# Optimization experiments

Measured on AMD Instinct MI355X. Metric: run time of the kernel, lower is better.

## Reference

```python
import jax, jax.numpy as jnp
import numpy as np
from jax import lax

RO = 4.0            # snake_config.ro (feature-map downsample ratio)
N_ADJ = 4           # snake_config.adj_num -> kernel = 2*4+1 = 9
K = 2 * N_ADJ + 1
DIL = (1, 1, 1, 2, 2, 4, 4)   # dilations of the 7 Snake residual circular convs
NMS_RADIUS = 2      # radius used in the iterative refinement cls_nms


def circ_conv(x, w, b, d):
    """Dilated circular conv along polygon axis. x:[N,C,P], w:[O,I,K]."""
    pad = N_ADJ * d
    xp = jnp.concatenate([x[..., -pad:], x, x[..., :pad]], axis=-1)
    y = lax.conv_general_dilated(xp, w, window_strides=(1,), padding='VALID',
                                 rhs_dilation=(d,),
                                 dimension_numbers=('NCH', 'OIH', 'NCH'))
    return y + b[None, :, None]


def conv1x1(x, w, b):
    # x:[N,C,P], w:[O,C] -> [N,O,P]
    return jnp.einsum('ncp,oc->nop', x, w) + b[None, :, None]


def bilinear_gather(cnn_feature, poly, ind):
    """grid_sample-style bilinear sampling (align_corners=False, zero pad).
    cnn_feature:[B,C,H,W], poly:[N,P,2] pixel coords, ind:[N] image index.
    Returns [N,C,P]."""
    B, C, H, W = cnn_feature.shape
    x = poly[..., 0] - 0.5
    y = poly[..., 1] - 0.5
    x0 = jnp.floor(x); y0 = jnp.floor(y)
    wx = x - x0; wy = y - y0
    x0i = x0.astype(jnp.int32); y0i = y0.astype(jnp.int32)

    def tap(yi, xi):
        valid = (xi >= 0) & (xi < W) & (yi >= 0) & (yi < H)
        xi_c = jnp.clip(xi, 0, W - 1)
        yi_c = jnp.clip(yi, 0, H - 1)
        f = cnn_feature[ind[:, None], :, yi_c, xi_c]  # [N,P,C]
        return f * valid[..., None]

    f00 = tap(y0i, x0i);     f01 = tap(y0i, x0i + 1)
    f10 = tap(y0i + 1, x0i); f11 = tap(y0i + 1, x0i + 1)
    out = (f00 * ((1 - wx) * (1 - wy))[..., None]
           + f01 * (wx * (1 - wy))[..., None]
           + f10 * ((1 - wx) * wy)[..., None]
           + f11 * (wx * wy)[..., None])
    return out.transpose(0, 2, 1)  # [N,C,P]


def cls_nms(cls, radius):
    """Circular local-max suppression of per-vertex scores. cls:[N,P,1]."""
    c = cls[..., 0]
    m = jnp.max(jnp.stack([jnp.roll(c, s, axis=1)
                           for s in range(-radius, radius + 1)], 0), axis=0)
    return jnp.where(c >= m, c, 0.0)[..., None]


def snake_body(x, head_w, head_b, res_w, res_b, fusion_w, fusion_b,
               pred1_w, pred1_b, pred2_w, pred2_b, pred3_w, pred3_b,
               cls1_w, cls1_b, cls2_w, cls2_b, cls3_w, cls3_b):
    h = jax.nn.relu(circ_conv(x, head_w, head_b, 1))
    states = [h]
    for i in range(7):  # fixed 7 residual layers, structurally distinct dilations
        r = jax.nn.relu(circ_conv(states[-1], res_w[i], res_b[i], DIL[i]))
        states.append(r + states[-1])
    state = jnp.concatenate(states, axis=1)                 # [N, 8*128, P]
    g = conv1x1(state, fusion_w, fusion_b)                  # [N, 256, P]
    g = jnp.max(g, axis=2, keepdims=True)
    g = jnp.broadcast_to(g, (state.shape[0], g.shape[1], state.shape[2]))
    state = jnp.concatenate([g, state], axis=1)             # [N, 1280, P]

    def head3(w1, b1, w2, b2, w3, b3):
        h1 = jax.nn.relu(conv1x1(state, w1, b1))
        h2 = jax.nn.relu(conv1x1(h1, w2, b2))
        return conv1x1(h2, w3, b3)

    offset = head3(pred1_w, pred1_b, pred2_w, pred2_b, pred3_w, pred3_b)  # [N,2,P]
    cls = head3(cls1_w, cls1_b, cls2_w, cls2_b, cls3_w, cls3_b)           # [N,1,P]
    return offset, cls


def setup_inputs() -> dict:
    key = jax.random.key(0)
    ks = jax.random.split(key, 32)
    B, C, H, W = 4, 64, 128, 128
    N, P = 512, 128
    SD = 128  # state_dim
    FD = 64 + 2 + 1  # feature_dim for iterative evolve_gcn
    std = 0.01  # conv init: normal(0, 0.01), bias 0 (matches module init)
    inp = {
        'cnn_feature': jax.random.normal(ks[0], (B, C, H, W), jnp.float32),
        'i_it_py': jax.random.uniform(ks[1], (N, P, 2), jnp.float32) * (W - 1),
        'c_it_py': jax.random.normal(ks[2], (N, P, 2), jnp.float32) * 0.2,
        'it_cls': jax.random.uniform(ks[3], (N, P), jnp.float32),
        'ind': jax.random.randint(ks[4], (N,), 0, B, jnp.int32),
        'head_w': jax.random.normal(ks[5], (SD, FD, K), jnp.float32) * std,
        'head_b': jnp.zeros((SD,), jnp.float32),
        'res_w': jax.random.normal(ks[6], (7, SD, SD, K), jnp.float32) * std,
        'res_b': jnp.zeros((7, SD), jnp.float32),
        'fusion_w': jax.random.normal(ks[7], (256, 8 * SD), jnp.float32) * std,
        'fusion_b': jnp.zeros((256,), jnp.float32),
        'pred1_w': jax.random.normal(ks[8], (256, 8 * SD + 256), jnp.float32) * std,
        'pred1_b': jnp.zeros((256,), jnp.float32),
        'pred2_w': jax.random.normal(ks[9], (64, 256), jnp.float32) * std,
        'pred2_b': jnp.zeros((64,), jnp.float32),
        'pred3_w': jax.random.normal(ks[10], (2, 64), jnp.float32) * std,
        'pred3_b': jnp.zeros((2,), jnp.float32),
        'cls1_w': jax.random.normal(ks[11], (256, 8 * SD + 256), jnp.float32) * std,
        'cls1_b': jnp.zeros((256,), jnp.float32),
        'cls2_w': jax.random.normal(ks[12], (64, 256), jnp.float32) * std,
        'cls2_b': jnp.zeros((64,), jnp.float32),
        'cls3_w': jax.random.normal(ks[13], (1, 64), jnp.float32) * std,
        'cls3_b': jnp.zeros((1,), jnp.float32),
    }
    return inp


def reference(cnn_feature, i_it_py, c_it_py, it_cls, ind,
              head_w, head_b, res_w, res_b, fusion_w, fusion_b,
              pred1_w, pred1_b, pred2_w, pred2_b, pred3_w, pred3_b,
              cls1_w, cls1_b, cls2_w, cls2_b, cls3_w, cls3_b):
    # evolve_poly: gather CNN features at vertices, concat scaled canonical
    # coords + per-vertex cls, run Snake, add offsets, NMS sigmoid scores.
    feat = bilinear_gather(cnn_feature, i_it_py, ind)        # [N,64,P]
    c = (c_it_py * RO).transpose(0, 2, 1)                    # [N,2,P]
    x = jnp.concatenate([feat, c, it_cls[:, None, :]], axis=1)  # [N,67,P]
    offset, cls = snake_body(x, head_w, head_b, res_w, res_b, fusion_w, fusion_b,
                             pred1_w, pred1_b, pred2_w, pred2_b, pred3_w, pred3_b,
                             cls1_w, cls1_b, cls2_w, cls2_b, cls3_w, cls3_b)
    i_poly = i_it_py * RO + offset.transpose(0, 2, 1)        # [N,P,2]
    cls = cls.transpose(0, 2, 1)                             # [N,P,1]
    nms = cls_nms(jax.nn.sigmoid(cls), NMS_RADIUS)           # [N,P,1]
    return i_poly, cls, nms
```

## Files before the change

kernel.cpp:

```cpp
#include <hip/hip_runtime.h>
#include <math.h>

typedef __attribute__((ext_vector_type(8))) short bf16x8;
typedef __attribute__((ext_vector_type(4))) float f32x4;

#define UOFF_CAW 0L
#define UOFF_FAW 2359296L
#define UOFF_H1W 2883584L
#define UOFF_W2F 3932160L
#define NB_TOT   3997696L
#define OFF_W1G  1998848L
#define OFF_GRAW 2129920L
#define OFF_DYN  2260992L
#define REPACK_N 4128768L

__device__ inline ushort f2bf_rne(float x) {
  uint u = __float_as_uint(x);
  return (ushort)((u + 0x7FFFu + ((u >> 16) & 1u)) >> 16);
}
__device__ inline void split_bf(float x, ushort& h, ushort& l) {
  uint u = __float_as_uint(x);
  uint hb = (u + 0x7FFFu + ((u >> 16) & 1u)) & 0xFFFF0000u;
  h = (ushort)(hb >> 16);
  l = f2bf_rne(x - __uint_as_float(hb));
}
__device__ inline ushort bfsel(float w, int split) {
  uint u = __float_as_uint(w);
  uint hb = (u + 0x7FFFu + ((u >> 16) & 1u)) & 0xFFFF0000u;
  if (split == 0) return (ushort)(hb >> 16);
  float lo = w - __uint_as_float(hb);
  uint ul = __float_as_uint(lo);
  return (ushort)((ul + 0x7FFFu + ((ul >> 16) & 1u)) >> 16);
}
__device__ inline bf16x8 asb(uint4 a) {
  union { uint4 u; bf16x8 v; } x; x.u = a; return x.v;
}
__device__ inline f32x4 MFMA_(bf16x8 a, bf16x8 b, f32x4 c) {
  return __builtin_amdgcn_mfma_f32_16x16x32_bf16(a, b, c, 0, 0, 0);
}
__device__ inline void bar_lgkm() {
  asm volatile("s_waitcnt lgkmcnt(0)" ::: "memory");
  __builtin_amdgcn_s_barrier();
}

__device__ inline void read_frag_pair(const char* xb, int pc, int g, int ic,
                                      bf16x8& bh, bf16x8& bl) {
  const int s0 = (pc & 7) << 4;
  const char* a = xb + pc * 512 + (((ic * 64 + (g << 4))) ^ s0);
  bh = asb(*(const uint4*)a);
  bl = asb(*(const uint4*)(a + 256));
}

__global__ void k_repack(const float* __restrict__ head_w, const float* __restrict__ res_w,
                         const float* __restrict__ fusion_w,
                         const float* __restrict__ pred1_w, const float* __restrict__ cls1_w,
                         const float* __restrict__ pred2_w, const float* __restrict__ cls2_w,
                         float* __restrict__ ws) {
  const long j = (long)blockIdx.x * 256 + threadIdx.x;
  if (j >= REPACK_N) return;
  if (j < NB_TOT) {
    ushort* wsu = (ushort*)ws;
    float w;
    if (j < UOFF_FAW) {
      int e = (int)(j & 7); long q = j >> 3;
      int lane = (int)(q & 63); q >>= 6;
      int mt = (int)(q & 1); q >>= 1;
      int split = (int)(q & 1); q >>= 1;
      int ic = (int)(q & 3); q >>= 2;
      int tap = (int)(q % 9); q /= 9;
      int mp = (int)(q & 3); int l = (int)(q >> 2);
      int gg = lane >> 4;
      int kl = (e < 4) ? (4 * gg + e) : (16 + 4 * gg + e - 4);
      int m = mp * 32 + mt * 16 + (lane & 15);
      int i = ic * 32 + kl;
      if (l == 0) w = (i < 67) ? head_w[((long)m * 67 + i) * 9 + tap] : 0.f;
      else        w = res_w[(((long)(l - 1) * 128 + m) * 128 + i) * 9 + tap];
      wsu[j] = bfsel(w, split);
    } else if (j < UOFF_H1W) {
      long jj = j - UOFF_FAW;
      int e = (int)(jj & 7); long q = jj >> 3;
      int lane = (int)(q & 63); q >>= 6;
      int mt = (int)(q & 1); q >>= 1;
      int split = (int)(q & 1); q >>= 1;
      int ic = (int)(q & 3); q >>= 2;
      int fm2 = (int)(q & 7); int l = (int)(q >> 3);
      int gg = lane >> 4;
      int kl = (e < 4) ? (4 * gg + e) : (16 + 4 * gg + e - 4);
      int m = fm2 * 32 + mt * 16 + (lane & 15);
      int i = ic * 32 + kl;
      w = fusion_w[(long)m * 1024 + l * 128 + i];
      wsu[j] = bfsel(w, split);
    } else if (j < UOFF_W2F) {
      long jj = j - UOFF_H1W;
      int e = (int)(jj & 7); long q = jj >> 3;
      int lane = (int)(q & 63); q >>= 6;
      int mt = (int)(q & 1); q >>= 1;
      int split = (int)(q & 1); q >>= 1;
      int ic = (int)(q & 3); q >>= 2;
      int slab = (int)(q & 7); q >>= 3;
      int mp = (int)(q & 7); int blk = (int)(q >> 3);
      int gg = lane >> 4;
      int kl = (e < 4) ? (4 * gg + e) : (16 + 4 * gg + e - 4);
      int m = blk * 256 + mp * 32 + mt * 16 + (lane & 15);
      int k = slab * 128 + ic * 32 + kl;
      w = (m < 256) ? pred1_w[(long)m * 1280 + 256 + k] : cls1_w[(long)(m - 256) * 1280 + 256 + k];
      wsu[j] = bfsel(w, split);
    } else {
      long jj = j - UOFF_W2F;
      int e = (int)(jj & 7); long q = jj >> 3;
      int lane = (int)(q & 63); q >>= 6;
      int split = (int)(q & 1); q >>= 1;
      int ic = (int)(q & 7); q >>= 3;
      int mfr = (int)(q & 3); int blk = (int)(q >> 2);
      int gg = lane >> 4;
      int kl = (e < 4) ? (4 * gg + e) : (16 + 4 * gg + e - 4);
      int m = mfr * 16 + (lane & 15);
      int k = ic * 32 + kl;
      w = blk ? cls2_w[(long)m * 256 + k] : pred2_w[(long)m * 256 + k];
      wsu[j] = bfsel(w, split);
    }
  } else {
    long q = j - NB_TOT; int o = (int)(q & 511); int c = (int)(q >> 9);
    ws[OFF_W1G + q] = (o < 256) ? pred1_w[(long)o * 1280 + c] : cls1_w[(long)(o - 256) * 1280 + c];
  }
}

__global__ __launch_bounds__(1024) __attribute__((amdgpu_waves_per_eu(4)))
void k_conv(const float* __restrict__ cnn, const float* __restrict__ i_it,
            const float* __restrict__ c_it, const float* __restrict__ cls_in,
            const int* __restrict__ ind,
            const ushort* __restrict__ CAW, const ushort* __restrict__ FAW,
            const float* __restrict__ head_b, const float* __restrict__ res_b,
            float* __restrict__ graw, float* __restrict__ states, int p0) {
  __shared__ uint4 xt4[4096];
  __shared__ float scr[512];
  char* xb = (char*)xt4;
  const int ln = blockIdx.x, n = p0 + ln, t = threadIdx.x;
  const int lane = t & 63, li = lane & 15, g = lane >> 4;
  const int wv = __builtin_amdgcn_readfirstlane(t >> 6);
  const int mp = wv & 3, np = wv >> 2;
  const int fm2 = wv & 7, fq = wv >> 3;

  {
    const int p = t & 127, qg = t >> 7;
    const long nb = (long)n * 128 + p;
    const int sw = p & 7;
    if (qg < 4) {
      const float gx = i_it[nb * 2 + 0] - 0.5f;
      const float gy = i_it[nb * 2 + 1] - 0.5f;
      const float fx = floorf(gx), fy = floorf(gy);
      const float wx = gx - fx, wy = gy - fy;
      const int x0 = (int)fx, y0 = (int)fy, x1 = x0 + 1, y1 = y0 + 1;
      const bool vx0 = (x0 >= 0) & (x0 < 128), vx1 = (x1 >= 0) & (x1 < 128);
      const bool vy0 = (y0 >= 0) & (y0 < 128), vy1 = (y1 >= 0) & (y1 < 128);
      const int x0c = min(max(x0, 0), 127), x1c = min(max(x1, 0), 127);
      const int y0c = min(max(y0, 0), 127), y1c = min(max(y1, 0), 127);
      const float w00 = (vx0 && vy0) ? (1.f - wx) * (1.f - wy) : 0.f;
      const float w01 = (vx1 && vy0) ? wx * (1.f - wy) : 0.f;
      const float w10 = (vx0 && vy1) ? (1.f - wx) * wy : 0.f;
      const float w11 = (vx1 && vy1) ? wx * wy : 0.f;
      const long base = (long)ind[n] * (64L * 16384);
      const int a00 = y0c * 128 + x0c, a01 = y0c * 128 + x1c;
      const int a10 = y1c * 128 + x0c, a11 = y1c * 128 + x1c;
#pragma unroll
      for (int qq = 0; qq < 4; qq++) {
        ushort hh[4], ll[4];
#pragma unroll
        for (int cc = 0; cc < 4; cc++) {
          const int c = qg * 16 + qq * 4 + cc;
          const float* f = cnn + base + (long)c * 16384;
          float x = f[a00] * w00 + f[a01] * w01 + f[a10] * w10 + f[a11] * w11;
          split_bf(x, hh[cc], ll[cc]);
        }
        const int G = ((qg >> 1) * 4 + qq) ^ sw;
        char* a = xb + p * 512 + G * 16 + (qg & 1) * 8;
        *(uint2*)a = make_uint2((uint)hh[0] | ((uint)hh[1] << 16), (uint)hh[2] | ((uint)hh[3] << 16));
        *(uint2*)(a + 256) = make_uint2((uint)ll[0] | ((uint)ll[1] << 16), (uint)ll[2] | ((uint)ll[3] << 16));
      }
    } else {
#pragma unroll
      for (int qq = 0; qq < 4; qq++) {
        ushort hh[4], ll[4];
        if (qg == 4 && qq == 0) {
          float v0 = c_it[nb * 2 + 0] * 4.f, v1 = c_it[nb * 2 + 1] * 4.f, v2 = cls_in[nb];
          split_bf(v0, hh[0], ll[0]); split_bf(v1, hh[1], ll[1]); split_bf(v2, hh[2], ll[2]);
          hh[3] = 0; ll[3] = 0;
        } else {
          hh[0] = hh[1] = hh[2] = hh[3] = 0; ll[0] = ll[1] = ll[2] = ll[3] = 0;
        }
        const int G = ((qg >> 1) * 4 + qq) ^ sw;
        char* a = xb + p * 512 + G * 16 + (qg & 1) * 8;
        *(uint2*)a = make_uint2((uint)hh[0] | ((uint)hh[1] << 16), (uint)hh[2] | ((uint)hh[3] << 16));
        *(uint2*)(a + 256) = make_uint2((uint)ll[0] | ((uint)ll[1] << 16), (uint)ll[2] | ((uint)ll[3] << 16));
      }
    }
  }
  __syncthreads();

  const f32x4 fz = {0.f, 0.f, 0.f, 0.f};
  f32x4 facc[2][4];
#pragma unroll
  for (int a = 0; a < 2; a++)
#pragma unroll
    for (int b = 0; b < 4; b++) facc[a][b] = fz;

  const uint4* caw = (const uint4*)CAW;
  const uint4* faw = (const uint4*)FAW;
  uint4* stq = (uint4*)(states + (long)ln * 131072);

  for (int l = 0; l < 8; l++) {
    const int dil = (l >= 6) ? 4 : ((l >= 4) ? 2 : 1);
    const int nic = (l == 0) ? 3 : 4;
    if (l > 0) {
      uint4* dst = stq + (long)(l - 1) * 4096;
#pragma unroll
      for (int k = 0; k < 4; k++) dst[k * 1024 + t] = xt4[k * 1024 + t];
      const uint4* fawl = faw + ((long)((l - 1) * 8 + fm2)) * 1024 + lane;
#pragma unroll
      for (int ic = 0; ic < 4; ic++) {
        const uint4* w0 = fawl + ic * 256;
        const bf16x8 Ah0 = asb(w0[0]),   Ah1 = asb(w0[64]);
        const bf16x8 Al0 = asb(w0[128]), Al1 = asb(w0[192]);
#pragma unroll
        for (int nt = 0; nt < 4; nt++) {
          const int pc = fq * 64 + nt * 16 + li;
          bf16x8 bh, bl;
          read_frag_pair(xb, pc, g, ic, bh, bl);
          facc[0][nt] = MFMA_(Ah0, bh, facc[0][nt]);
          facc[1][nt] = MFMA_(Ah1, bh, facc[1][nt]);
          facc[0][nt] = MFMA_(Ah0, bl, facc[0][nt]);
          facc[1][nt] = MFMA_(Ah1, bl, facc[1][nt]);
          facc[0][nt] = MFMA_(Al0, bh, facc[0][nt]);
          facc[1][nt] = MFMA_(Al1, bh, facc[1][nt]);
        }
      }
    }
    f32x4 cacc[2][2];
    cacc[0][0] = fz; cacc[0][1] = fz; cacc[1][0] = fz; cacc[1][1] = fz;
    const uint4* cawl = caw + ((long)(l * 4 + mp)) * 9216;
    for (int tap = 0; tap < 9; tap++) {
      const int shift = (tap - 4) * dil;
      const int pc0 = (np * 32 + li + shift + 128) & 127;
      const int pc1 = (np * 32 + 16 + li + shift + 128) & 127;
      const uint4* cawt = cawl + tap * 1024 + lane;
      for (int ic = 0; ic < nic; ic++) {
        bf16x8 bh0, bl0, bh1, bl1;
        read_frag_pair(xb, pc0, g, ic, bh0, bl0);
        read_frag_pair(xb, pc1, g, ic, bh1, bl1);
        const uint4* w0 = cawt + ic * 256;
        const bf16x8 Ah0 = asb(w0[0]),   Ah1 = asb(w0[64]);
        const bf16x8 Al0 = asb(w0[128]), Al1 = asb(w0[192]);
        cacc[0][0] = MFMA_(Ah0, bh0, cacc[0][0]);
        cacc[0][1] = MFMA_(Ah0, bh1, cacc[0][1]);
        cacc[1][0] = MFMA_(Ah1, bh0, cacc[1][0]);
        cacc[1][1] = MFMA_(Ah1, bh1, cacc[1][1]);
        cacc[0][0] = MFMA_(Ah0, bl0, cacc[0][0]);
        cacc[0][1] = MFMA_(Ah0, bl1, cacc[0][1]);
        cacc[1][0] = MFMA_(Ah1, bl0, cacc[1][0]);
        cacc[1][1] = MFMA_(Ah1, bl1, cacc[1][1]);
        cacc[0][0] = MFMA_(Al0, bh0, cacc[0][0]);
        cacc[0][1] = MFMA_(Al0, bh1, cacc[0][1]);
        cacc[1][0] = MFMA_(Al1, bh0, cacc[1][0]);
        cacc[1][1] = MFMA_(Al1, bh1, cacc[1][1]);
      }
    }
    bar_lgkm();
    {
      const float* bsrc = (l == 0) ? head_b : (res_b + (l - 1) * 128);
      const float4 b0 = *(const float4*)&bsrc[mp * 32 + g * 4];
      const float4 b1 = *(const float4*)&bsrc[mp * 32 + 16 + g * 4];
#pragma unroll
      for (int nt = 0; nt < 2; nt++) {
        const int p = np * 32 + nt * 16 + li;
        const int X = (mp * 64 + g * 16) ^ ((p & 7) << 4);
        char* a = xb + p * 512 + X;
        float v[8];
        v[0] = fmaxf(cacc[0][nt][0] + b0.x, 0.f);
        v[1] = fmaxf(cacc[0][nt][1] + b0.y, 0.f);
        v[2] = fmaxf(cacc[0][nt][2] + b0.z, 0.f);
        v[3] = fmaxf(cacc[0][nt][3] + b0.w, 0.f);
        v[4] = fmaxf(cacc[1][nt][0] + b1.x, 0.f);
        v[5] = fmaxf(cacc[1][nt][1] + b1.y, 0.f);
        v[6] = fmaxf(cacc[1][nt][2] + b1.z, 0.f);
        v[7] = fmaxf(cacc[1][nt][3] + b1.w, 0.f);
        if (l > 0) {
          const uint4 oh = *(const uint4*)a;
          const uint4 ol = *(const uint4*)(a + 256);
          const uint hw[4] = {oh.x, oh.y, oh.z, oh.w};
          const uint lw[4] = {ol.x, ol.y, ol.z, ol.w};
#pragma unroll
          for (int k = 0; k < 8; k++) {
            const uint hh = (k & 1) ? (hw[k >> 1] & 0xFFFF0000u) : ((hw[k >> 1] & 0xFFFFu) << 16);
            const uint ll = (k & 1) ? (lw[k >> 1] & 0xFFFF0000u) : ((lw[k >> 1] & 0xFFFFu) << 16);
            v[k] += __uint_as_float(hh) + __uint_as_float(ll);
          }
        }
        ushort hh[8], ll[8];
#pragma unroll
        for (int k = 0; k < 8; k++) split_bf(v[k], hh[k], ll[k]);
        *(uint4*)a = make_uint4((uint)hh[0] | ((uint)hh[1] << 16), (uint)hh[2] | ((uint)hh[3] << 16),
                                (uint)hh[4] | ((uint)hh[5] << 16), (uint)hh[6] | ((uint)hh[7] << 16));
        *(uint4*)(a + 256) = make_uint4((uint)ll[0] | ((uint)ll[1] << 16), (uint)ll[2] | ((uint)ll[3] << 16),
                                        (uint)ll[4] | ((uint)ll[5] << 16), (uint)ll[6] | ((uint)ll[7] << 16));
      }
    }
    __syncthreads();
  }

  {
    uint4* dst = stq + 7L * 4096;
#pragma unroll
    for (int k = 0; k < 4; k++) dst[k * 1024 + t] = xt4[k * 1024 + t];
    const uint4* fawl = faw + ((long)(7 * 8 + fm2)) * 1024 + lane;
#pragma unroll
    for (int ic = 0; ic < 4; ic++) {
      const uint4* w0 = fawl + ic * 256;
      const bf16x8 Ah0 = asb(w0[0]),   Ah1 = asb(w0[64]);
      const bf16x8 Al0 = asb(w0[128]), Al1 = asb(w0[192]);
#pragma unroll
      for (int nt = 0; nt < 4; nt++) {
        const int pc = fq * 64 + nt * 16 + li;
        bf16x8 bh, bl;
        read_frag_pair(xb, pc, g, ic, bh, bl);
        facc[0][nt] = MFMA_(Ah0, bh, facc[0][nt]);
        facc[1][nt] = MFMA_(Ah1, bh, facc[1][nt]);
        facc[0][nt] = MFMA_(Ah0, bl, facc[0][nt]);
        facc[1][nt] = MFMA_(Ah1, bl, facc[1][nt]);
        facc[0][nt] = MFMA_(Al0, bh, facc[0][nt]);
        facc[1][nt] = MFMA_(Al1, bh, facc[1][nt]);
      }
    }
  }

#pragma unroll
  for (int mt = 0; mt < 2; mt++) {
#pragma unroll
    for (int r = 0; r < 4; r++) {
      float m = fmaxf(fmaxf(facc[mt][0][r], facc[mt][1][r]),
                      fmaxf(facc[mt][2][r], facc[mt][3][r]));
#pragma unroll
      for (int s = 1; s < 16; s <<= 1) m = fmaxf(m, __shfl_xor(m, s, 64));
      if (li == 0) scr[(fm2 * 32 + mt * 16 + g * 4 + r) * 2 + fq] = m;
    }
  }
  bar_lgkm();
  if (t < 256) graw[(long)n * 256 + t] = fmaxf(scr[2 * t], scr[2 * t + 1]);
}

__global__ __launch_bounds__(1024) __attribute__((amdgpu_waves_per_eu(4)))
void k_h1t(const float* __restrict__ states, const ushort* __restrict__ H1W,
           const ushort* __restrict__ W2F,
           const float* __restrict__ graw, const float* __restrict__ fus_b,
           const float* __restrict__ W1G, const float* __restrict__ p1b, const float* __restrict__ c1b,
           const float* __restrict__ p2b, const float* __restrict__ c2b,
           const float* __restrict__ p3w, const float* __restrict__ p3b,
           const float* __restrict__ c3w, const float* __restrict__ c3b,
           const float* __restrict__ i_it, float* __restrict__ out, int p0) {
  __shared__ uint4 xt4[4096];
  __shared__ float sg[256];
  __shared__ float hg_s[256];
  char* xb = (char*)xt4;
  const int b = blockIdx.x, ln = b >> 1, blk = b & 1, t = threadIdx.x;
  const int n = p0 + ln;
  const int lane = t & 63, li = lane & 15, g = lane >> 4;
  const int wv = __builtin_amdgcn_readfirstlane(t >> 6);
  const int mw = wv & 7, qw = wv >> 3;
  const uint4* sp = (const uint4*)(states + (long)ln * 131072);
  const uint4* aw = (const uint4*)H1W;
  const uint4* w2 = (const uint4*)W2F;
  const f32x4 fz = {0.f, 0.f, 0.f, 0.f};

  uint4 stg[4];
#pragma unroll
  for (int k = 0; k < 4; k++) stg[k] = sp[k * 1024 + t];

  if (t < 256) sg[t] = graw[(long)n * 256 + t] + fus_b[t];
  __syncthreads();
  if (t < 256) {
    float s = blk ? c1b[t] : p1b[t];
    const float* w = W1G + blk * 256 + t;
#pragma unroll 8
    for (int c = 0; c < 256; c++) s = fmaf(w[(long)c * 512], sg[c], s);
    hg_s[t] = s;
  }

  f32x4 acc[2][4];
#pragma unroll
  for (int a = 0; a < 2; a++)
#pragma unroll
    for (int c = 0; c < 4; c++) acc[a][c] = fz;

  for (int s = 0; s < 8; s++) {
#pragma unroll
    for (int k = 0; k < 4; k++) xt4[k * 1024 + t] = stg[k];
    bar_lgkm();
    if (s < 7) {
#pragma unroll
      for (int k = 0; k < 4; k++) stg[k] = sp[(s + 1) * 4096 + k * 1024 + t];
    }
    const uint4* awl = aw + (((long)(blk * 8 + mw)) * 8 + s) * 1024 + lane;
#pragma unroll
    for (int ic = 0; ic < 4; ic++) {
      const uint4* w0 = awl + ic * 256;
      const bf16x8 Ah0 = asb(w0[0]),   Ah1 = asb(w0[64]);
      const bf16x8 Al0 = asb(w0[128]), Al1 = asb(w0[192]);
#pragma unroll
      for (int nt = 0; nt < 4; nt++) {
        const int pc = qw * 64 + nt * 16 + li;
        bf16x8 bh, bl;
        read_frag_pair(xb, pc, g, ic, bh, bl);
        acc[0][nt] = MFMA_(Ah0, bh, acc[0][nt]);
        acc[1][nt] = MFMA_(Ah1, bh, acc[1][nt]);
        acc[0][nt] = MFMA_(Ah0, bl, acc[0][nt]);
        acc[1][nt] = MFMA_(Ah1, bl, acc[1][nt]);
        acc[0][nt] = MFMA_(Al0, bh, acc[0][nt]);
        acc[1][nt] = MFMA_(Al1, bh, acc[1][nt]);
      }
    }
    bar_lgkm();
  }

  const float4 hq0 = *(const float4*)&hg_s[mw * 32 + g * 4];
  const float4 hq1 = *(const float4*)&hg_s[mw * 32 + 16 + g * 4];
#pragma unroll
  for (int nt = 0; nt < 4; nt++) {
    acc[0][nt][0] = fmaxf(acc[0][nt][0] + hq0.x, 0.f);
    acc[0][nt][1] = fmaxf(acc[0][nt][1] + hq0.y, 0.f);
    acc[0][nt][2] = fmaxf(acc[0][nt][2] + hq0.z, 0.f);
    acc[0][nt][3] = fmaxf(acc[0][nt][3] + hq0.w, 0.f);
    acc[1][nt][0] = fmaxf(acc[1][nt][0] + hq1.x, 0.f);
    acc[1][nt][1] = fmaxf(acc[1][nt][1] + hq1.y, 0.f);
    acc[1][nt][2] = fmaxf(acc[1][nt][2] + hq1.z, 0.f);
    acc[1][nt][3] = fmaxf(acc[1][nt][3] + hq1.w, 0.f);
  }

  const int mfr = wv & 3, nfr = wv >> 2;
  const float* b2 = blk ? c2b : p2b;
  f32x4 a2s[2];
#pragma unroll
  for (int h = 0; h < 2; h++) {
    bar_lgkm();
    if (qw == h) {
#pragma unroll
      for (int nt = 0; nt < 4; nt++) {
        const int pl = nt * 16 + li;
        char* a = xb + pl * 1024 + ((mw * 64 + g * 16) ^ ((pl & 7) << 4));
        ushort hh[8], ll[8];
#pragma unroll
        for (int e = 0; e < 4; e++) { split_bf(acc[0][nt][e], hh[e], ll[e]); }
#pragma unroll
        for (int e = 0; e < 4; e++) { split_bf(acc[1][nt][e], hh[4 + e], ll[4 + e]); }
        *(uint4*)a = make_uint4((uint)hh[0] | ((uint)hh[1] << 16), (uint)hh[2] | ((uint)hh[3] << 16),
                                (uint)hh[4] | ((uint)hh[5] << 16), (uint)hh[6] | ((uint)hh[7] << 16));
        *(uint4*)(a + 512) = make_uint4((uint)ll[0] | ((uint)ll[1] << 16), (uint)ll[2] | ((uint)ll[3] << 16),
                                        (uint)ll[4] | ((uint)ll[5] << 16), (uint)ll[6] | ((uint)ll[7] << 16));
      }
    }
    bar_lgkm();
    a2s[h] = fz;
    {
      const int pl = nfr * 16 + li;
#pragma unroll
      for (int ic = 0; ic < 8; ic++) {
        const uint4* wb = w2 + (((long)(blk * 4 + mfr) * 8 + ic) * 2) * 64 + lane;
        const bf16x8 Ah = asb(wb[0]), Al = asb(wb[64]);
        const char* ba = xb + pl * 1024 + ((ic * 64 + g * 16) ^ ((pl & 7) << 4));
        const bf16x8 bh = asb(*(const uint4*)ba);
        const bf16x8 bl = asb(*(const uint4*)(ba + 512));
        a2s[h] = MFMA_(Ah, bh, a2s[h]);
        a2s[h] = MFMA_(Ah, bl, a2s[h]);
        a2s[h] = MFMA_(Al, bh, a2s[h]);
      }
    }
  }
  bar_lgkm();

  {
    float* h2L = (float*)xb;
    const int jl = mfr * 16 + g * 4;
#pragma unroll
    for (int h = 0; h < 2; h++) {
      const int pos = h * 64 + nfr * 16 + li;
      h2L[(jl + 0) * 128 + pos] = fmaxf(a2s[h][0] + b2[jl + 0], 0.f);
      h2L[(jl + 1) * 128 + pos] = fmaxf(a2s[h][1] + b2[jl + 1], 0.f);
      h2L[(jl + 2) * 128 + pos] = fmaxf(a2s[h][2] + b2[jl + 2], 0.f);
      h2L[(jl + 3) * 128 + pos] = fmaxf(a2s[h][3] + b2[jl + 3], 0.f);
    }
  }
  bar_lgkm();

  {
    const float* h2L = (const float*)xb;
    const int pp = t & 127;
    if (blk == 0) {
      if (t < 128) {
        float o0v = p3b[0], o1v = p3b[1];
        for (int j = 0; j < 64; j++) {
          const float hp = h2L[j * 128 + pp];
          o0v = fmaf(p3w[j], hp, o0v);
          o1v = fmaf(p3w[64 + j], hp, o1v);
        }
        const long ip = ((long)n * 128 + pp) * 2;
        out[ip + 0] = i_it[ip + 0] * 4.f + o0v;
        out[ip + 1] = i_it[ip + 1] * 4.f + o1v;
      }
    } else {
      float sig = 0.f;
      if (t < 128) {
        float cv = c3b[0];
        for (int j = 0; j < 64; j++) cv = fmaf(c3w[j], h2L[j * 128 + pp], cv);
        out[131072 + (long)n * 128 + pp] = cv;
        sig = 1.f / (1.f + expf(-cv));
        sg[pp] = sig;
      }
      bar_lgkm();
      if (t < 128) {
        float m = sg[pp];
#pragma unroll
        for (int s = 1; s <= 2; s++) {
          m = fmaxf(m, sg[(pp + s) & 127]);
          m = fmaxf(m, sg[(pp + 128 - s) & 127]);
        }
        out[196608 + (long)n * 128 + pp] = (sig >= m) ? sig : 0.f;
      }
    }
  }
}

extern "C" void kernel_launch(void* const* d_in, const int* in_sizes, int n_in,
                              void* d_out, int out_size, void* d_ws, size_t ws_size,
                              hipStream_t stream) {
  const float* cnn      = (const float*)d_in[0];
  const float* i_it     = (const float*)d_in[1];
  const float* c_it     = (const float*)d_in[2];
  const float* it_cls   = (const float*)d_in[3];
  const int*   ind      = (const int*)d_in[4];
  const float* head_w   = (const float*)d_in[5];
  const float* head_b   = (const float*)d_in[6];
  const float* res_w    = (const float*)d_in[7];
  const float* res_b    = (const float*)d_in[8];
  const float* fusion_w = (const float*)d_in[9];
  const float* fusion_b = (const float*)d_in[10];
  const float* pred1_w  = (const float*)d_in[11];
  const float* pred1_b  = (const float*)d_in[12];
  const float* pred2_w  = (const float*)d_in[13];
  const float* pred2_b  = (const float*)d_in[14];
  const float* pred3_w  = (const float*)d_in[15];
  const float* pred3_b  = (const float*)d_in[16];
  const float* cls1_w   = (const float*)d_in[17];
  const float* cls1_b   = (const float*)d_in[18];
  const float* cls2_w   = (const float*)d_in[19];
  const float* cls2_b   = (const float*)d_in[20];
  const float* cls3_w   = (const float*)d_in[21];
  const float* cls3_b   = (const float*)d_in[22];
  float* ws = (float*)d_ws;
  float* out = (float*)d_out;
  const ushort* wsu = (const ushort*)d_ws;

  k_repack<<<(int)((REPACK_N + 255) / 256), 256, 0, stream>>>(
      head_w, res_w, fusion_w, pred1_w, cls1_w, pred2_w, cls2_w, ws);

  long avail_f = (long)(ws_size / 4) - OFF_DYN;
  long Cl = avail_f / 131072;
  int C = (Cl >= 512) ? 512 : ((Cl >= 256) ? 256 : (int)(Cl < 1 ? 1 : Cl));
  float* states = ws + OFF_DYN;

  for (int p0 = 0; p0 < 512; p0 += C) {
    int Cc = (512 - p0 < C) ? (512 - p0) : C;
    k_conv<<<Cc, 1024, 0, stream>>>(cnn, i_it, c_it, it_cls, ind,
                                    wsu + UOFF_CAW, wsu + UOFF_FAW, head_b, res_b,
                                    ws + OFF_GRAW, states, p0);
    k_h1t<<<2 * Cc, 1024, 0, stream>>>(states, wsu + UOFF_H1W, wsu + UOFF_W2F,
                                       ws + OFF_GRAW, fusion_b, ws + OFF_W1G,
                                       pred1_b, cls1_b, pred2_b, cls2_b,
                                       pred3_w, pred3_b, cls3_w, cls3_b,
                                       i_it, out, p0);
  }
}
```

Measured before the change: 1.022 ms.

## Merge pred/cls head blocks per polygon and double-buffer state tiles in LDS

The head kernel now runs one 1024-thread block per polygon that computes both the pred and cls branches, instead of two blocks per polygon. Each state tile is then loaded from global memory and staged in LDS once and reused by both branches. State staging is double-buffered in LDS, so the next slice is written while the current one is consumed, which removes one barrier per step. In exchange, LDS per block doubles to 128KB and each wave holds twice as many accumulators, which can lower occupancy and raise register pressure; the grid also has half as many blocks.

```diff
diff --git a/kernel.cpp b/kernel.cpp
--- a/kernel.cpp
+++ b/kernel.cpp
@@ -356,15 +356,13 @@
            const float* __restrict__ p3w, const float* __restrict__ p3b,
            const float* __restrict__ c3w, const float* __restrict__ c3b,
            const float* __restrict__ i_it, float* __restrict__ out, int p0) {
-  __shared__ uint4 xt4[4096];
+  __shared__ uint4 xt4[8192];
   __shared__ float sg[256];
-  __shared__ float hg_s[256];
+  __shared__ float hg_s[512];
   char* xb = (char*)xt4;
-  const int b = blockIdx.x, ln = b >> 1, blk = b & 1, t = threadIdx.x;
-  const int n = p0 + ln;
+  const int ln = blockIdx.x, n = p0 + ln, t = threadIdx.x;
   const int lane = t & 63, li = lane & 15, g = lane >> 4;
   const int wv = __builtin_amdgcn_readfirstlane(t >> 6);
-  const int mw = wv & 7, qw = wv >> 3;
   const uint4* sp = (const uint4*)(states + (long)ln * 131072);
   const uint4* aw = (const uint4*)H1W;
   const uint4* w2 = (const uint4*)W2F;
@@ -375,40 +373,41 @@
   for (int k = 0; k < 4; k++) stg[k] = sp[k * 1024 + t];
 
   if (t < 256) sg[t] = graw[(long)n * 256 + t] + fus_b[t];
-  __syncthreads();
-  if (t < 256) {
-    float s = blk ? c1b[t] : p1b[t];
-    const float* w = W1G + blk * 256 + t;
+  bar_lgkm();
+#pragma unroll
+  for (int k = 0; k < 4; k++) xt4[k * 1024 + t] = stg[k];
+  if (t < 512) {
+    float s = (t < 256) ? p1b[t] : c1b[t - 256];
+    const float* w = W1G + t;
 #pragma unroll 8
     for (int c = 0; c < 256; c++) s = fmaf(w[(long)c * 512], sg[c], s);
     hg_s[t] = s;
   }
-
-  f32x4 acc[2][4];
+  bar_lgkm();
+
+  f32x4 acc[2][8];
 #pragma unroll
   for (int a = 0; a < 2; a++)
 #pragma unroll
-    for (int c = 0; c < 4; c++) acc[a][c] = fz;
+    for (int c = 0; c < 8; c++) acc[a][c] = fz;
 
   for (int s = 0; s < 8; s++) {
-#pragma unroll
-    for (int k = 0; k < 4; k++) xt4[k * 1024 + t] = stg[k];
-    bar_lgkm();
     if (s < 7) {
 #pragma unroll
-      for (int k = 0; k < 4; k++) stg[k] = sp[(s + 1) * 4096 + k * 1024 + t];
-    }
-    const uint4* awl = aw + (((long)(blk * 8 + mw)) * 8 + s) * 1024 + lane;
+      for (int k = 0; k < 4; k++) stg[k] = sp[(long)(s + 1) * 4096 + k * 1024 + t];
+    }
+    const char* xc = xb + (s & 1) * 65536;
+    const uint4* awl = aw + ((long)(wv * 8 + s)) * 1024 + lane;
 #pragma unroll
     for (int ic = 0; ic < 4; ic++) {
       const uint4* w0 = awl + ic * 256;
       const bf16x8 Ah0 = asb(w0[0]),   Ah1 = asb(w0[64]);
       const bf16x8 Al0 = asb(w0[128]), Al1 = asb(w0[192]);
 #pragma unroll
-      for (int nt = 0; nt < 4; nt++) {
-        const int pc = qw * 64 + nt * 16 + li;
+      for (int nt = 0; nt < 8; nt++) {
+        const int pc = nt * 16 + li;
         bf16x8 bh, bl;
-        read_frag_pair(xb, pc, g, ic, bh, bl);
+        read_frag_pair(xc, pc, g, ic, bh, bl);
         acc[0][nt] = MFMA_(Ah0, bh, acc[0][nt]);
         acc[1][nt] = MFMA_(Ah1, bh, acc[1][nt]);
         acc[0][nt] = MFMA_(Ah0, bl, acc[0][nt]);
@@ -417,13 +416,18 @@
         acc[1][nt] = MFMA_(Al1, bh, acc[1][nt]);
       }
     }
+    if (s < 7) {
+      uint4* dbuf = xt4 + ((s + 1) & 1) * 4096;
+#pragma unroll
+      for (int k = 0; k < 4; k++) dbuf[k * 1024 + t] = stg[k];
+    }
     bar_lgkm();
   }
 
-  const float4 hq0 = *(const float4*)&hg_s[mw * 32 + g * 4];
-  const float4 hq1 = *(const float4*)&hg_s[mw * 32 + 16 + g * 4];
-#pragma unroll
-  for (int nt = 0; nt < 4; nt++) {
+  const float4 hq0 = *(const float4*)&hg_s[wv * 32 + g * 4];
+  const float4 hq1 = *(const float4*)&hg_s[wv * 32 + 16 + g * 4];
+#pragma unroll
+  for (int nt = 0; nt < 8; nt++) {
     acc[0][nt][0] = fmaxf(acc[0][nt][0] + hq0.x, 0.f);
     acc[0][nt][1] = fmaxf(acc[0][nt][1] + hq0.y, 0.f);
     acc[0][nt][2] = fmaxf(acc[0][nt][2] + hq0.z, 0.f);
@@ -434,57 +438,59 @@
     acc[1][nt][3] = fmaxf(acc[1][nt][3] + hq1.w, 0.f);
   }
 
-  const int mfr = wv & 3, nfr = wv >> 2;
-  const float* b2 = blk ? c2b : p2b;
-  f32x4 a2s[2];
-#pragma unroll
-  for (int h = 0; h < 2; h++) {
+  const int mf = wv >> 1, nf = wv & 1;
+  const int blkc = mf >> 2, mfr = mf & 3;
+  f32x4 a2q[4];
+#pragma unroll
+  for (int q = 0; q < 4; q++) {
+#pragma unroll
+    for (int mt = 0; mt < 2; mt++) {
+#pragma unroll
+      for (int ntl = 0; ntl < 2; ntl++) {
+        const int nt = 2 * q + ntl;
+        const int pl = ntl * 16 + li;
+        char* a = xb + pl * 2048 + ((wv * 64 + g * 16) ^ ((pl & 7) << 4)) + mt * 8;
+        ushort hh[4], llw[4];
+        split_bf(acc[mt][nt][0], hh[0], llw[0]);
+        split_bf(acc[mt][nt][1], hh[1], llw[1]);
+        split_bf(acc[mt][nt][2], hh[2], llw[2]);
+        split_bf(acc[mt][nt][3], hh[3], llw[3]);
+        *(uint2*)a = make_uint2((uint)hh[0] | ((uint)hh[1] << 16), (uint)hh[2] | ((uint)hh[3] << 16));
+        *(uint2*)(a + 1024) = make_uint2((uint)llw[0] | ((uint)llw[1] << 16), (uint)llw[2] | ((uint)llw[3] << 16));
+      }
+    }
     bar_lgkm();
-    if (qw == h) {
-#pragma unroll
-      for (int nt = 0; nt < 4; nt++) {
-        const int pl = nt * 16 + li;
-        char* a = xb + pl * 1024 + ((mw * 64 + g * 16) ^ ((pl & 7) << 4));
-        ushort hh[8], ll[8];
-#pragma unroll
-        for (int e = 0; e < 4; e++) { split_bf(acc[0][nt][e], hh[e], ll[e]); }
-#pragma unroll
-        for (int e = 0; e < 4; e++) { split_bf(acc[1][nt][e], hh[4 + e], ll[4 + e]); }
-        *(uint4*)a = make_uint4((uint)hh[0] | ((uint)hh[1] << 16), (uint)hh[2] | ((uint)hh[3] << 16),
-                                (uint)hh[4] | ((uint)hh[5] << 16), (uint)hh[6] | ((uint)hh[7] << 16));
-        *(uint4*)(a + 512) = make_uint4((uint)ll[0] | ((uint)ll[1] << 16), (uint)ll[2] | ((uint)ll[3] << 16),
-                                        (uint)ll[4] | ((uint)ll[5] << 16), (uint)ll[6] | ((uint)ll[7] << 16));
+    a2q[q] = fz;
+    {
+      const int pl = nf * 16 + li;
+#pragma unroll
+      for (int ic = 0; ic < 8; ic++) {
+        const int kc = blkc * 8 + ic;
+        const uint4* wb = w2 + (((long)(blkc * 4 + mfr) * 8 + ic) * 2) * 64 + lane;
+        const bf16x8 Ah = asb(wb[0]), Al = asb(wb[64]);
+        const char* ba = xb + pl * 2048 + ((kc * 64 + g * 16) ^ ((pl & 7) << 4));
+        const bf16x8 bh = asb(*(const uint4*)ba);
+        const bf16x8 bl = asb(*(const uint4*)(ba + 1024));
+        a2q[q] = MFMA_(Ah, bh, a2q[q]);
+        a2q[q] = MFMA_(Ah, bl, a2q[q]);
+        a2q[q] = MFMA_(Al, bh, a2q[q]);
       }
     }
     bar_lgkm();
-    a2s[h] = fz;
-    {
-      const int pl = nfr * 16 + li;
-#pragma unroll
-      for (int ic = 0; ic < 8; ic++) {
-        const uint4* wb = w2 + (((long)(blk * 4 + mfr) * 8 + ic) * 2) * 64 + lane;
-        const bf16x8 Ah = asb(wb[0]), Al = asb(wb[64]);
-        const char* ba = xb + pl * 1024 + ((ic * 64 + g * 16) ^ ((pl & 7) << 4));
-        const bf16x8 bh = asb(*(const uint4*)ba);
-        const bf16x8 bl = asb(*(const uint4*)(ba + 512));
-        a2s[h] = MFMA_(Ah, bh, a2s[h]);
-        a2s[h] = MFMA_(Ah, bl, a2s[h]);
-        a2s[h] = MFMA_(Al, bh, a2s[h]);
-      }
-    }
-  }
-  bar_lgkm();
+  }
 
   {
     float* h2L = (float*)xb;
-    const int jl = mfr * 16 + g * 4;
-#pragma unroll
-    for (int h = 0; h < 2; h++) {
-      const int pos = h * 64 + nfr * 16 + li;
-      h2L[(jl + 0) * 128 + pos] = fmaxf(a2s[h][0] + b2[jl + 0], 0.f);
-      h2L[(jl + 1) * 128 + pos] = fmaxf(a2s[h][1] + b2[jl + 1], 0.f);
-      h2L[(jl + 2) * 128 + pos] = fmaxf(a2s[h][2] + b2[jl + 2], 0.f);
-      h2L[(jl + 3) * 128 + pos] = fmaxf(a2s[h][3] + b2[jl + 3], 0.f);
+    const int row0 = mf * 16 + g * 4;
+    const float4 b2v = (mf < 4) ? *(const float4*)&p2b[row0]
+                                : *(const float4*)&c2b[row0 - 64];
+#pragma unroll
+    for (int q = 0; q < 4; q++) {
+      const int pos = q * 32 + nf * 16 + li;
+      h2L[(row0 + 0) * 128 + pos] = fmaxf(a2q[q][0] + b2v.x, 0.f);
+      h2L[(row0 + 1) * 128 + pos] = fmaxf(a2q[q][1] + b2v.y, 0.f);
+      h2L[(row0 + 2) * 128 + pos] = fmaxf(a2q[q][2] + b2v.z, 0.f);
+      h2L[(row0 + 3) * 128 + pos] = fmaxf(a2q[q][3] + b2v.w, 0.f);
     }
   }
   bar_lgkm();
@@ -492,37 +498,32 @@
   {
     const float* h2L = (const float*)xb;
     const int pp = t & 127;
-    if (blk == 0) {
-      if (t < 128) {
-        float o0v = p3b[0], o1v = p3b[1];
-        for (int j = 0; j < 64; j++) {
-          const float hp = h2L[j * 128 + pp];
-          o0v = fmaf(p3w[j], hp, o0v);
-          o1v = fmaf(p3w[64 + j], hp, o1v);
-        }
-        const long ip = ((long)n * 128 + pp) * 2;
-        out[ip + 0] = i_it[ip + 0] * 4.f + o0v;
-        out[ip + 1] = i_it[ip + 1] * 4.f + o1v;
-      }
-    } else {
-      float sig = 0.f;
-      if (t < 128) {
-        float cv = c3b[0];
-        for (int j = 0; j < 64; j++) cv = fmaf(c3w[j], h2L[j * 128 + pp], cv);
-        out[131072 + (long)n * 128 + pp] = cv;
-        sig = 1.f / (1.f + expf(-cv));
-        sg[pp] = sig;
-      }
-      bar_lgkm();
-      if (t < 128) {
-        float m = sg[pp];
-#pragma unroll
-        for (int s = 1; s <= 2; s++) {
-          m = fmaxf(m, sg[(pp + s) & 127]);
-          m = fmaxf(m, sg[(pp + 128 - s) & 127]);
-        }
-        out[196608 + (long)n * 128 + pp] = (sig >= m) ? sig : 0.f;
-      }
+    float sig = 0.f;
+    if (t < 128) {
+      float o0v = p3b[0], o1v = p3b[1], cv = c3b[0];
+      for (int j = 0; j < 64; j++) {
+        const float hp = h2L[j * 128 + pp];
+        const float hc = h2L[(64 + j) * 128 + pp];
+        o0v = fmaf(p3w[j], hp, o0v);
+        o1v = fmaf(p3w[64 + j], hp, o1v);
+        cv = fmaf(c3w[j], hc, cv);
+      }
+      const long ip = ((long)n * 128 + pp) * 2;
+      out[ip + 0] = i_it[ip + 0] * 4.f + o0v;
+      out[ip + 1] = i_it[ip + 1] * 4.f + o1v;
+      out[131072 + (long)n * 128 + pp] = cv;
+      sig = 1.f / (1.f + expf(-cv));
+      sg[pp] = sig;
+    }
+    bar_lgkm();
+    if (t < 128) {
+      float m = sg[pp];
+#pragma unroll
+      for (int s = 1; s <= 2; s++) {
+        m = fmaxf(m, sg[(pp + s) & 127]);
+        m = fmaxf(m, sg[(pp + 128 - s) & 127]);
+      }
+      out[196608 + (long)n * 128 + pp] = (sig >= m) ? sig : 0.f;
     }
   }
 }
@@ -570,10 +571,10 @@
     k_conv<<<Cc, 1024, 0, stream>>>(cnn, i_it, c_it, it_cls, ind,
                                     wsu + UOFF_CAW, wsu + UOFF_FAW, head_b, res_b,
                                     ws + OFF_GRAW, states, p0);
-    k_h1t<<<2 * Cc, 1024, 0, stream>>>(states, wsu + UOFF_H1W, wsu + UOFF_W2F,
-                                       ws + OFF_GRAW, fusion_b, ws + OFF_W1G,
-                                       pred1_b, cls1_b, pred2_b, cls2_b,
-                                       pred3_w, pred3_b, cls3_w, cls3_b,
-                                       i_it, out, p0);
-  }
-}
+    k_h1t<<<Cc, 1024, 0, stream>>>(states, wsu + UOFF_H1W, wsu + UOFF_W2F,
+                                   ws + OFF_GRAW, fusion_b, ws + OFF_W1G,
+                                   pred1_b, cls1_b, pred2_b, cls2_b,
+                                   pred3_w, pred3_b, cls3_w, cls3_b,
+                                   i_it, out, p0);
+  }
+}
```

New measurement: 925.7 us. 1.1x faster.
